# Kernel tuning notes

Hardware: AMD Instinct MI355X
Metric: run time of the kernel (lower is better)

Reference implementation:

```python
import jax, jax.numpy as jnp
import numpy as np

N = 40000      # nodes
E = 640000     # edges (before self-loops)
G = 64         # graphs in batch
H = 4          # heads
C = 64         # channels per head (graph_hidden_channels)
F_IN = 256     # num_node_features
NHID = 1024
NOUT = 768
NEG_SLOPE = 0.2


def setup_inputs() -> dict:
    key = jax.random.key(0)
    ks = jax.random.split(key, 20)
    s = 0.05
    inp = {
        "x": jax.random.normal(ks[0], (N, F_IN), jnp.float32),
        "edge_index": jax.random.randint(ks[1], (2, E), 0, N, dtype=jnp.int64),
        "batch": jnp.sort(jax.random.randint(ks[2], (N,), 0, G, dtype=jnp.int64)),
        # GATConv 1: in F_IN -> H heads x C
        "W1": jax.random.normal(ks[3], (F_IN, H * C), jnp.float32) * s,
        "as1": jax.random.normal(ks[4], (H, C), jnp.float32) * s,
        "ad1": jax.random.normal(ks[5], (H, C), jnp.float32) * s,
        "b1": jnp.zeros((H * C,), jnp.float32),
        # GATConv 2: in H*C -> H x C
        "W2": jax.random.normal(ks[6], (H * C, H * C), jnp.float32) * s,
        "as2": jax.random.normal(ks[7], (H, C), jnp.float32) * s,
        "ad2": jax.random.normal(ks[8], (H, C), jnp.float32) * s,
        "b2": jnp.zeros((H * C,), jnp.float32),
        # GATConv 3
        "W3": jax.random.normal(ks[9], (H * C, H * C), jnp.float32) * s,
        "as3": jax.random.normal(ks[10], (H, C), jnp.float32) * s,
        "ad3": jax.random.normal(ks[11], (H, C), jnp.float32) * s,
        "b3": jnp.zeros((H * C,), jnp.float32),
        # MLP head
        "Wm1": jax.random.normal(ks[12], (H * C, NHID), jnp.float32) * s,
        "bm1": jnp.zeros((NHID,), jnp.float32),
        "Wm2": jax.random.normal(ks[13], (NHID, NOUT), jnp.float32) * s,
        "bm2": jnp.zeros((NOUT,), jnp.float32),
    }
    return inp


def _gat_layer(x, src, dst, W, a_src, a_dst, b):
    """PyG GATConv (concat=True, self-loops already in src/dst)."""
    n = x.shape[0]
    h = (x @ W).reshape(n, H, C)                       # [N,H,C]
    # per-node attention scalars (gather scalars per edge, not full features)
    alpha_src = jnp.einsum('nhc,hc->nh', h, a_src)     # [N,H]
    alpha_dst = jnp.einsum('nhc,hc->nh', h, a_dst)     # [N,H]
    e = alpha_src[src] + alpha_dst[dst]                # [E,H]
    e = jax.nn.leaky_relu(e, NEG_SLOPE)
    # segment softmax over incoming edges of each dst node
    m = jax.ops.segment_max(e, dst, num_segments=n)    # [N,H]
    e = jnp.exp(e - m[dst])
    denom = jax.ops.segment_sum(e, dst, num_segments=n)  # [N,H]; >0 via self-loops
    alpha = e / denom[dst]                             # [E,H]
    # scatter-add weighted source features to destinations
    msg = h[src] * alpha[:, :, None]                   # [E,H,C]
    out = jax.ops.segment_sum(msg, dst, num_segments=n)  # [N,H,C]
    return out.reshape(n, H * C) + b


def reference(x, edge_index, batch,
              W1, as1, ad1, b1,
              W2, as2, ad2, b2,
              W3, as3, ad3, b3,
              Wm1, bm1, Wm2, bm2):
    n = x.shape[0]
    loops = jnp.arange(n, dtype=edge_index.dtype)
    src = jnp.concatenate([edge_index[0], loops])
    dst = jnp.concatenate([edge_index[1], loops])

    h = jax.nn.relu(_gat_layer(x, src, dst, W1, as1, ad1, b1))
    h = jax.nn.relu(_gat_layer(h, src, dst, W2, as2, ad2, b2))
    h = _gat_layer(h, src, dst, W3, as3, ad3, b3)

    # global mean pool over graphs
    sums = jax.ops.segment_sum(h, batch, num_segments=G)      # [G, H*C]
    counts = jax.ops.segment_sum(jnp.ones((n,), h.dtype), batch, num_segments=G)
    pooled = sums / jnp.maximum(counts, 1.0)[:, None]

    out = jax.nn.relu(pooled @ Wm1 + bm1)
    out = out @ Wm2 + bm2
    return out
```

## Files before the change

kernel.cpp:

```cpp
#include <hip/hip_runtime.h>
#include <hip/hip_bf16.h>
#include <math.h>

#define N_NODES 40000
#define N_EDGES 640000
#define N_GRAPH 64
#define HEADS 4
#define CHAN 64
#define HC 256
#define NHID 1024
#define NOUT 768
#define E_TOT (N_EDGES + N_NODES)
#define SCAN_NB ((N_NODES + 255) / 256)

typedef __attribute__((ext_vector_type(8))) short bf16x8;
typedef __attribute__((ext_vector_type(4))) float f32x4;

__device__ inline float bflo(unsigned u) { return __uint_as_float(u << 16); }
__device__ inline float bfhi(unsigned u) { return __uint_as_float(u & 0xffff0000u); }

__device__ inline unsigned bfbits(float f) {
    __hip_bfloat16 b = __float2bfloat16(f);
    return (unsigned)*reinterpret_cast<unsigned short*>(&b);
}
__device__ inline unsigned pk2bf(float lo, float hi) {
    return bfbits(lo) | (bfbits(hi) << 16);
}


__global__ void conv_wt3_kernel(const float* __restrict__ W1, const float* __restrict__ W2,
                                const float* __restrict__ W3, __hip_bfloat16* __restrict__ T1,
                                __hip_bfloat16* __restrict__ T2, __hip_bfloat16* __restrict__ T3) {
    const float* W = (blockIdx.y == 0) ? W1 : (blockIdx.y == 1) ? W2 : W3;
    __hip_bfloat16* T = (blockIdx.y == 0) ? T1 : (blockIdx.y == 1) ? T2 : T3;
    int k = blockIdx.x, n = threadIdx.x;
    T[(size_t)n * 256 + k] = __float2bfloat16(W[(size_t)k * 256 + n]);
}


__global__ void count_deg_kernel(const int* __restrict__ ei, int* __restrict__ deg) {
    int i = blockIdx.x * blockDim.x + threadIdx.x;
    if (i >= E_TOT) return;
    int dst = (i < N_EDGES) ? ei[N_EDGES + i] : (i - N_EDGES);
    atomicAdd(&deg[dst], 1);
}

__global__ __launch_bounds__(256)
void scan_p1_kernel(const int* __restrict__ deg, int* __restrict__ bsum) {
    const int b = blockIdx.x, t = threadIdx.x;
    const int i = b * 256 + t;
    int v = (i < N_NODES) ? deg[i] : 0;
    #pragma unroll
    for (int off = 1; off < 64; off <<= 1) v += __shfl_xor(v, off, 64);
    __shared__ int ws[4];
    if ((t & 63) == 0) ws[t >> 6] = v;
    __syncthreads();
    if (t == 0) bsum[b] = ws[0] + ws[1] + ws[2] + ws[3];
}

__global__ __launch_bounds__(256)
void scan_p2_kernel(int* __restrict__ bsum) {
    __shared__ int s[256];
    const int t = threadIdx.x;
    int v = (t < SCAN_NB) ? bsum[t] : 0;
    s[t] = v;
    __syncthreads();
    #pragma unroll
    for (int off = 1; off < 256; off <<= 1) {
        int x = (t >= off) ? s[t - off] : 0;
        __syncthreads();
        s[t] += x;
        __syncthreads();
    }
    if (t < SCAN_NB) bsum[t] = s[t] - v;
}

__global__ __launch_bounds__(256)
void scan_p3_kernel(const int* __restrict__ deg, const int* __restrict__ bsum,
                    int* __restrict__ rowptr) {
    __shared__ int s[256];
    const int b = blockIdx.x, t = threadIdx.x;
    const int i = b * 256 + t;
    int v = (i < N_NODES) ? deg[i] : 0;
    s[t] = v;
    __syncthreads();
    #pragma unroll
    for (int off = 1; off < 256; off <<= 1) {
        int x = (t >= off) ? s[t - off] : 0;
        __syncthreads();
        s[t] += x;
        __syncthreads();
    }
    if (i < N_NODES) rowptr[i] = bsum[b] + s[t] - v;
    if (i == 0) rowptr[N_NODES] = E_TOT;
}

__global__ void fill_csr_kernel(const int* __restrict__ ei, const int* __restrict__ rowptr,
                                int* __restrict__ cursor, int* __restrict__ csr_src) {
    int i = blockIdx.x * blockDim.x + threadIdx.x;
    if (i >= E_TOT) return;
    int src, dst;
    if (i < N_EDGES) { src = ei[i]; dst = ei[N_EDGES + i]; }
    else             { src = dst = i - N_EDGES; }
    int pos = atomicAdd(&cursor[dst], 1);
    csr_src[rowptr[dst] + pos] = src;
}


template<int CAST>
__global__ __launch_bounds__(256)
void gemm_mfma_kernel(const void* __restrict__ Ain, const __hip_bfloat16* __restrict__ Wt,
                      __hip_bfloat16* __restrict__ C,
                      const float* __restrict__ a_s, const float* __restrict__ a_d,
                      float* __restrict__ asrc, float* __restrict__ adst) {
    __shared__ __align__(16) union {
        struct { ushort A0[32][32]; ushort B0[256][32]; ushort A1[32][32]; ushort B1[256][32]; } t;
        float strip[4][16][68];
    } lds;

    const int tid = threadIdx.x;
    const int lane = tid & 63;
    const int l15 = lane & 15, lq = lane >> 4;
    const int wc  = tid >> 6;
    const int row0 = blockIdx.x * 32;
    const char* Wb = (const char*)Wt;
    const int br = tid >> 2;
    const int bq = tid & 3;

    f32x4 acc[2][4];
    #pragma unroll
    for (int m = 0; m < 2; m++)
        #pragma unroll
        for (int n = 0; n < 4; n++)
            acc[m][n] = (f32x4){0.f, 0.f, 0.f, 0.f};

    {
        #pragma unroll
        for (int c = 0; c < 4; c++) {
            uint4 v = *reinterpret_cast<const uint4*>(Wb + (size_t)(c * 64 + br) * 512 + bq * 16);
            *reinterpret_cast<uint4*>(&lds.t.B0[c * 64 + br][bq * 8]) = v;
        }
        if (CAST) {
            const float* Af = (const float*)Ain;
            float4 v = *reinterpret_cast<const float4*>(&Af[(size_t)(row0 + (tid >> 3)) * 256 + (tid & 7) * 4]);
            uint2 w = make_uint2(pk2bf(v.x, v.y), pk2bf(v.z, v.w));
            *reinterpret_cast<uint2*>((ushort*)lds.t.A0 + tid * 4) = w;
        } else if (tid < 128) {
            const char* Ab = (const char*)Ain;
            uint4 v = *reinterpret_cast<const uint4*>(Ab + (size_t)(row0 + (tid >> 2)) * 512 + (tid & 3) * 16);
            *reinterpret_cast<uint4*>((ushort*)lds.t.A0 + tid * 8) = v;
        }
        __syncthreads();
    }

    for (int kt = 0; kt < 8; ++kt) {
        ushort (*Acur)[32] = (kt & 1) ? lds.t.A1 : lds.t.A0;
        ushort (*Bcur)[32] = (kt & 1) ? lds.t.B1 : lds.t.B0;
        bf16x8 af[2], bfr[4];
        #pragma unroll
        for (int m = 0; m < 2; m++)
            af[m] = *reinterpret_cast<const bf16x8*>(&Acur[m * 16 + l15][lq * 8]);
        #pragma unroll
        for (int n = 0; n < 4; n++)
            bfr[n] = *reinterpret_cast<const bf16x8*>(&Bcur[wc * 64 + n * 16 + l15][lq * 8]);
        uint4 rb0, rb1, rb2, rb3, ra; float4 rf;
        if (kt < 7) {
            const size_t ko = (size_t)(kt + 1) * 64;
            rb0 = *reinterpret_cast<const uint4*>(Wb + (size_t)(      br) * 512 + bq * 16 + ko);
            rb1 = *reinterpret_cast<const uint4*>(Wb + (size_t)( 64 + br) * 512 + bq * 16 + ko);
            rb2 = *reinterpret_cast<const uint4*>(Wb + (size_t)(128 + br) * 512 + bq * 16 + ko);
            rb3 = *reinterpret_cast<const uint4*>(Wb + (size_t)(192 + br) * 512 + bq * 16 + ko);
            if (CAST) {
                const float* Af = (const float*)Ain;
                rf = *reinterpret_cast<const float4*>(&Af[(size_t)(row0 + (tid >> 3)) * 256 + (kt + 1) * 32 + (tid & 7) * 4]);
            } else if (tid < 128) {
                const char* Ab = (const char*)Ain;
                ra = *reinterpret_cast<const uint4*>(Ab + (size_t)(row0 + (tid >> 2)) * 512 + (tid & 3) * 16 + ko);
            }
        }
        #pragma unroll
        for (int m = 0; m < 2; m++)
            #pragma unroll
            for (int n = 0; n < 4; n++)
                acc[m][n] = __builtin_amdgcn_mfma_f32_16x16x32_bf16(af[m], bfr[n], acc[m][n], 0, 0, 0);
        if (kt < 7) {
            ushort (*Anx)[32] = (kt & 1) ? lds.t.A0 : lds.t.A1;
            ushort (*Bnx)[32] = (kt & 1) ? lds.t.B0 : lds.t.B1;
            *reinterpret_cast<uint4*>(&Bnx[      br][bq * 8]) = rb0;
            *reinterpret_cast<uint4*>(&Bnx[ 64 + br][bq * 8]) = rb1;
            *reinterpret_cast<uint4*>(&Bnx[128 + br][bq * 8]) = rb2;
            *reinterpret_cast<uint4*>(&Bnx[192 + br][bq * 8]) = rb3;
            if (CAST) {
                uint2 w = make_uint2(pk2bf(rf.x, rf.y), pk2bf(rf.z, rf.w));
                *reinterpret_cast<uint2*>((ushort*)Anx + tid * 4) = w;
            } else if (tid < 128) {
                *reinterpret_cast<uint4*>((ushort*)Anx + tid * 8) = ra;
            }
            __syncthreads();
        }
    }

    const int head = wc;
    const int r  = lane >> 2;
    const int cq = lane & 3;
    #pragma unroll
    for (int m = 0; m < 2; m++) {
        #pragma unroll
        for (int n = 0; n < 4; n++)
            #pragma unroll
            for (int reg = 0; reg < 4; reg++)
                lds.strip[wc][lq * 4 + reg][n * 16 + l15] = acc[m][n][reg];
        f32x4 c0 = *reinterpret_cast<const f32x4*>(&lds.strip[wc][r][cq * 16]);
        f32x4 c1 = *reinterpret_cast<const f32x4*>(&lds.strip[wc][r][cq * 16 + 4]);
        f32x4 c2 = *reinterpret_cast<const f32x4*>(&lds.strip[wc][r][cq * 16 + 8]);
        f32x4 c3 = *reinterpret_cast<const f32x4*>(&lds.strip[wc][r][cq * 16 + 12]);
        float ps = 0.f, pd = 0.f;
        #pragma unroll
        for (int k4 = 0; k4 < 4; k4++) {
            f32x4 cv = (k4 == 0) ? c0 : (k4 == 1) ? c1 : (k4 == 2) ? c2 : c3;
            #pragma unroll
            for (int j = 0; j < 4; j++) {
                ps = fmaf(cv[j], a_s[head * 64 + cq * 16 + k4 * 4 + j], ps);
                pd = fmaf(cv[j], a_d[head * 64 + cq * 16 + k4 * 4 + j], pd);
            }
        }
        ps += __shfl_xor(ps, 1, 4); ps += __shfl_xor(ps, 2, 4);
        pd += __shfl_xor(pd, 1, 4); pd += __shfl_xor(pd, 2, 4);
        const int row = row0 + m * 16 + r;
        if (cq == 0) {
            asrc[row * 4 + head] = ps;
            adst[row * 4 + head] = pd;
        }
        uint4 o0 = make_uint4(pk2bf(c0[0], c0[1]), pk2bf(c0[2], c0[3]),
                              pk2bf(c1[0], c1[1]), pk2bf(c1[2], c1[3]));
        uint4 o1 = make_uint4(pk2bf(c2[0], c2[1]), pk2bf(c2[2], c2[3]),
                              pk2bf(c3[0], c3[1]), pk2bf(c3[2], c3[3]));
        __hip_bfloat16* Cp = C + (size_t)row * 256 + wc * 64 + cq * 16;
        *reinterpret_cast<uint4*>(Cp) = o0;
        *reinterpret_cast<uint4*>(Cp + 8) = o1;
    }
}


#define ACHUNK 256

__global__ __launch_bounds__(256)
void gat_fused_agg(const __hip_bfloat16* __restrict__ h, const float* __restrict__ asrc,
                   const float* __restrict__ adst, const int* __restrict__ rowptr,
                   const int* __restrict__ csr_src, const float* __restrict__ bias,
                   __hip_bfloat16* __restrict__ out, int do_relu) {
    __shared__ int   s_src[ACHUNK];
    __shared__ float s_w[ACHUNK][5];
    __shared__ float s_acc[8][HC];
    __shared__ float s_sum[4];

    const int n = blockIdx.x;
    const int t = threadIdx.x;
    const int lane = t & 63;
    const int wid = t >> 6;
    const int grp = t >> 5;
    const int gl  = t & 31;
    const int h3  = gl >> 3;
    const int start = rowptr[n];
    const int deg = rowptr[n + 1] - start;
    const float ad = adst[n * 4 + wid];

    float ssum = 0.f;
    float acc[8] = {0.f, 0.f, 0.f, 0.f, 0.f, 0.f, 0.f, 0.f};

    for (int c0 = 0; c0 < deg; c0 += ACHUNK) {
        const int cn = min(ACHUNK, deg - c0);
        if (c0) __syncthreads();
        for (int e = lane; e < cn; e += 64) {
            int src = csr_src[start + c0 + e];
            if (wid == 0) s_src[e] = src;
            float sc = asrc[src * 4 + wid] + ad;
            sc = (sc >= 0.f) ? sc : 0.2f * sc;
            float w = __expf(sc);
            s_w[e][wid] = w;
            ssum += w;
        }
        __syncthreads();
        #pragma unroll 2
        for (int e = grp; e < cn; e += 8) {
            float w = s_w[e][h3];
            uint4 v = *reinterpret_cast<const uint4*>(&h[(size_t)s_src[e] * HC + gl * 8]);
            acc[0] = fmaf(w, bflo(v.x), acc[0]);
            acc[1] = fmaf(w, bfhi(v.x), acc[1]);
            acc[2] = fmaf(w, bflo(v.y), acc[2]);
            acc[3] = fmaf(w, bfhi(v.y), acc[3]);
            acc[4] = fmaf(w, bflo(v.z), acc[4]);
            acc[5] = fmaf(w, bfhi(v.z), acc[5]);
            acc[6] = fmaf(w, bflo(v.w), acc[6]);
            acc[7] = fmaf(w, bfhi(v.w), acc[7]);
        }
    }
    #pragma unroll
    for (int off = 1; off < 64; off <<= 1) ssum += __shfl_xor(ssum, off, 64);
    if (lane == 0) s_sum[wid] = ssum;
    *reinterpret_cast<float4*>(&s_acc[grp][gl * 8])     = make_float4(acc[0], acc[1], acc[2], acc[3]);
    *reinterpret_cast<float4*>(&s_acc[grp][gl * 8 + 4]) = make_float4(acc[4], acc[5], acc[6], acc[7]);
    __syncthreads();
    float tot = 0.f;
    #pragma unroll
    for (int g = 0; g < 8; g++) tot += s_acc[g][t];
    float r = tot / s_sum[t >> 6] + bias[t];
    if (do_relu) r = fmaxf(r, 0.f);
    out[(size_t)n * HC + t] = __float2bfloat16(r);
}


__global__ __launch_bounds__(1024)
void pool_mlp1_kernel(const __hip_bfloat16* __restrict__ h, const int* __restrict__ batch,
                      const float* __restrict__ Wm1, const float* __restrict__ bm1,
                      float* __restrict__ hidden) {
    __shared__ float s_part[4][256];
    __shared__ float row[256];
    const int g = blockIdx.x, t = threadIdx.x;
    int lo = 0, hi = N_NODES;
    while (lo < hi) { int mid = (lo + hi) >> 1; if (batch[mid] < g) lo = mid + 1; else hi = mid; }
    const int start = lo;
    lo = 0; hi = N_NODES;
    while (lo < hi) { int mid = (lo + hi) >> 1; if (batch[mid] < g + 1) lo = mid + 1; else hi = mid; }
    const int end = lo;

    const int sub = t >> 8, ch = t & 255;
    float a = 0.f;
    for (int n = start + sub; n < end; n += 4)
        a += __bfloat162float(h[(size_t)n * HC + ch]);
    s_part[sub][ch] = a;
    __syncthreads();
    if (t < 256) {
        float c = (float)max(end - start, 1);
        row[t] = (s_part[0][t] + s_part[1][t] + s_part[2][t] + s_part[3][t]) / c;
    }
    __syncthreads();
    float acc = bm1[t];
    for (int k = 0; k < 256; k++) acc = fmaf(row[k], Wm1[(size_t)k * NHID + t], acc);
    hidden[(size_t)g * NHID + t] = fmaxf(acc, 0.f);
}

__global__ __launch_bounds__(768)
void mlp2_kernel(const float* __restrict__ hidden, const float* __restrict__ W,
                 const float* __restrict__ b, float* __restrict__ out) {
    __shared__ float row[NHID];
    const int g = blockIdx.x, t = threadIdx.x;
    row[t] = hidden[g * NHID + t];
    if (t < NHID - NOUT) row[NOUT + t] = hidden[g * NHID + NOUT + t];
    __syncthreads();
    float acc = b[t];
    for (int k = 0; k < NHID; k++) acc = fmaf(row[k], W[(size_t)k * NOUT + t], acc);
    out[g * NOUT + t] = acc;
}


extern "C" void kernel_launch(void* const* d_in, const int* in_sizes, int n_in,
                              void* d_out, int out_size, void* d_ws, size_t ws_size,
                              hipStream_t stream) {
    const float* x  = (const float*)d_in[0];
    const int* ei   = (const int*)d_in[1];
    const int* batch = (const int*)d_in[2];
    const float* W1 = (const float*)d_in[3];
    const float* as1 = (const float*)d_in[4];
    const float* ad1 = (const float*)d_in[5];
    const float* b1 = (const float*)d_in[6];
    const float* W2 = (const float*)d_in[7];
    const float* as2 = (const float*)d_in[8];
    const float* ad2 = (const float*)d_in[9];
    const float* b2 = (const float*)d_in[10];
    const float* W3 = (const float*)d_in[11];
    const float* as3 = (const float*)d_in[12];
    const float* ad3 = (const float*)d_in[13];
    const float* b3 = (const float*)d_in[14];
    const float* Wm1 = (const float*)d_in[15];
    const float* bm1 = (const float*)d_in[16];
    const float* Wm2 = (const float*)d_in[17];
    const float* bm2 = (const float*)d_in[18];
    float* out = (float*)d_out;

    char* base = (char*)d_ws;
    size_t off = 0;
    auto alloc = [&](size_t bytes) { char* p = base + off; off = (off + bytes + 255) & ~(size_t)255; return p; };
    __hip_bfloat16* hA   = (__hip_bfloat16*)alloc((size_t)N_NODES * 256 * 2);
    __hip_bfloat16* hB   = (__hip_bfloat16*)alloc((size_t)N_NODES * 256 * 2);
    __hip_bfloat16* Wt1  = (__hip_bfloat16*)alloc((size_t)256 * 256 * 2);
    __hip_bfloat16* Wt2  = (__hip_bfloat16*)alloc((size_t)256 * 256 * 2);
    __hip_bfloat16* Wt3  = (__hip_bfloat16*)alloc((size_t)256 * 256 * 2);
    float* asrc   = (float*)alloc((size_t)N_NODES * 4 * 4);
    float* adst   = (float*)alloc((size_t)N_NODES * 4 * 4);
    int*   deg    = (int*)alloc((size_t)N_NODES * 4);
    int*   cursor = (int*)alloc((size_t)N_NODES * 4);
    int*   rowptr = (int*)alloc((size_t)(N_NODES + 1) * 4);
    int*   bsum   = (int*)alloc((size_t)SCAN_NB * 4);
    int*   csrsrc = (int*)alloc((size_t)E_TOT * 4);
    float* hidden = (float*)alloc((size_t)N_GRAPH * NHID * 4);
    (void)ws_size; (void)n_in; (void)in_sizes; (void)out_size;

    hipMemsetAsync(deg, 0, (size_t)N_NODES * 4 * 2, stream);

    conv_wt3_kernel<<<dim3(256, 3), 256, 0, stream>>>(W1, W2, W3, Wt1, Wt2, Wt3);

    const int eb = (E_TOT + 255) / 256;
    count_deg_kernel<<<eb, 256, 0, stream>>>(ei, deg);
    scan_p1_kernel<<<SCAN_NB, 256, 0, stream>>>(deg, bsum);
    scan_p2_kernel<<<1, 256, 0, stream>>>(bsum);
    scan_p3_kernel<<<SCAN_NB, 256, 0, stream>>>(deg, bsum, rowptr);
    fill_csr_kernel<<<eb, 256, 0, stream>>>(ei, rowptr, cursor, csrsrc);

    const int ggrid = N_NODES / 32;

    gemm_mfma_kernel<1><<<ggrid, 256, 0, stream>>>(x, Wt1, hA, as1, ad1, asrc, adst);
    gat_fused_agg<<<N_NODES, 256, 0, stream>>>(hA, asrc, adst, rowptr, csrsrc, b1, hB, 1);
    gemm_mfma_kernel<0><<<ggrid, 256, 0, stream>>>(hB, Wt2, hA, as2, ad2, asrc, adst);
    gat_fused_agg<<<N_NODES, 256, 0, stream>>>(hA, asrc, adst, rowptr, csrsrc, b2, hB, 1);
    gemm_mfma_kernel<0><<<ggrid, 256, 0, stream>>>(hB, Wt3, hA, as3, ad3, asrc, adst);
    gat_fused_agg<<<N_NODES, 256, 0, stream>>>(hA, asrc, adst, rowptr, csrsrc, b3, hB, 0);

    pool_mlp1_kernel<<<N_GRAPH, 1024, 0, stream>>>(hB, batch, Wm1, bm1, hidden);
    mlp2_kernel<<<N_GRAPH, NOUT, 0, stream>>>(hidden, Wm2, bm2, out);
}
```

Measured before the change: 422.1 us.

## Keep weight slice in registers and stream A rows directly in GEMM

The node-feature GEMM is restructured so each 512-thread block loads a 128-column weight slice once into swizzled LDS and then into registers, covering two heads. Each wave streams 16-row A tiles straight from global memory into registers with a prefetch of the next tile, with no per-k LDS staging and no __syncthreads in the main loop. The attention dot products are computed from MFMA outputs with cross-lane shuffles instead of an LDS transpose. The aim is to cut LDS traffic and synchronization, at the cost of heavy register pressure (64 B fragments per lane) and a small grid of 250 blocks.

```diff
diff --git a/kernel.cpp b/kernel.cpp
--- a/kernel.cpp
+++ b/kernel.cpp
@@ -108,136 +108,122 @@
 
 
 template<int CAST>
-__global__ __launch_bounds__(256)
+__global__ __launch_bounds__(512, 2)
 void gemm_mfma_kernel(const void* __restrict__ Ain, const __hip_bfloat16* __restrict__ Wt,
                       __hip_bfloat16* __restrict__ C,
                       const float* __restrict__ a_s, const float* __restrict__ a_d,
                       float* __restrict__ asrc, float* __restrict__ adst) {
-    __shared__ __align__(16) union {
-        struct { ushort A0[32][32]; ushort B0[256][32]; ushort A1[32][32]; ushort B1[256][32]; } t;
-        float strip[4][16][68];
-    } lds;
+    __shared__ ushort Wl[128 * 256];
 
     const int tid = threadIdx.x;
     const int lane = tid & 63;
     const int l15 = lane & 15, lq = lane >> 4;
-    const int wc  = tid >> 6;
-    const int row0 = blockIdx.x * 32;
-    const char* Wb = (const char*)Wt;
-    const int br = tid >> 2;
-    const int bq = tid & 3;
-
-    f32x4 acc[2][4];
-    #pragma unroll
-    for (int m = 0; m < 2; m++)
-        #pragma unroll
-        for (int n = 0; n < 4; n++)
-            acc[m][n] = (f32x4){0.f, 0.f, 0.f, 0.f};
+    const int w = tid >> 6;
+    const int hsel = w >> 2;
+    const int stripe = w & 3;
+    const int head = blockIdx.y * 2 + hsel;
+    const int row_base = blockIdx.x * 320;
 
     {
-        #pragma unroll
-        for (int c = 0; c < 4; c++) {
-            uint4 v = *reinterpret_cast<const uint4*>(Wb + (size_t)(c * 64 + br) * 512 + bq * 16);
-            *reinterpret_cast<uint4*>(&lds.t.B0[c * 64 + br][bq * 8]) = v;
-        }
+        const int col = tid >> 2;
+        const char* Wb = (const char*)(Wt + (size_t)(blockIdx.y * 128 + col) * 256);
+        #pragma unroll
+        for (int j = 0; j < 8; j++) {
+            int q = (tid & 3) * 8 + j;
+            uint4 v = *reinterpret_cast<const uint4*>(Wb + q * 16);
+            *reinterpret_cast<uint4*>(&Wl[col * 256 + ((q ^ (col & 7)) * 8)]) = v;
+        }
+    }
+    __syncthreads();
+
+    bf16x8 b[8][4];
+    #pragma unroll
+    for (int kt = 0; kt < 8; kt++)
+        #pragma unroll
+        for (int n = 0; n < 4; n++) {
+            int cl = hsel * 64 + n * 16 + l15;
+            int q = kt * 4 + lq;
+            b[kt][n] = *reinterpret_cast<const bf16x8*>(&Wl[cl * 256 + ((q ^ (cl & 7)) * 8)]);
+        }
+
+    float was[4], wad[4];
+    #pragma unroll
+    for (int n = 0; n < 4; n++) {
+        was[n] = a_s[head * 64 + n * 16 + l15];
+        wad[n] = a_d[head * 64 + n * 16 + l15];
+    }
+
+    auto loadA = [&](int T, bf16x8* a) {
+        const int row = row_base + T * 16 + l15;
         if (CAST) {
             const float* Af = (const float*)Ain;
-            float4 v = *reinterpret_cast<const float4*>(&Af[(size_t)(row0 + (tid >> 3)) * 256 + (tid & 7) * 4]);
-            uint2 w = make_uint2(pk2bf(v.x, v.y), pk2bf(v.z, v.w));
-            *reinterpret_cast<uint2*>((ushort*)lds.t.A0 + tid * 4) = w;
-        } else if (tid < 128) {
-            const char* Ab = (const char*)Ain;
-            uint4 v = *reinterpret_cast<const uint4*>(Ab + (size_t)(row0 + (tid >> 2)) * 512 + (tid & 3) * 16);
-            *reinterpret_cast<uint4*>((ushort*)lds.t.A0 + tid * 8) = v;
-        }
-        __syncthreads();
-    }
-
-    for (int kt = 0; kt < 8; ++kt) {
-        ushort (*Acur)[32] = (kt & 1) ? lds.t.A1 : lds.t.A0;
-        ushort (*Bcur)[32] = (kt & 1) ? lds.t.B1 : lds.t.B0;
-        bf16x8 af[2], bfr[4];
-        #pragma unroll
-        for (int m = 0; m < 2; m++)
-            af[m] = *reinterpret_cast<const bf16x8*>(&Acur[m * 16 + l15][lq * 8]);
+            #pragma unroll
+            for (int kt = 0; kt < 8; kt++) {
+                float4 u0 = *reinterpret_cast<const float4*>(&Af[(size_t)row * 256 + kt * 32 + lq * 8]);
+                float4 u1 = *reinterpret_cast<const float4*>(&Af[(size_t)row * 256 + kt * 32 + lq * 8 + 4]);
+                uint4 uv = make_uint4(pk2bf(u0.x, u0.y), pk2bf(u0.z, u0.w),
+                                      pk2bf(u1.x, u1.y), pk2bf(u1.z, u1.w));
+                a[kt] = *reinterpret_cast<bf16x8*>(&uv);
+            }
+        } else {
+            const __hip_bfloat16* Ab = (const __hip_bfloat16*)Ain;
+            #pragma unroll
+            for (int kt = 0; kt < 8; kt++) {
+                uint4 uv = *reinterpret_cast<const uint4*>(&Ab[(size_t)row * 256 + kt * 32 + lq * 8]);
+                a[kt] = *reinterpret_cast<bf16x8*>(&uv);
+            }
+        }
+    };
+
+    bf16x8 aA[8], aB[8];
+    loadA(stripe, aA);
+    #pragma unroll
+    for (int ti = 0; ti < 5; ti++) {
+        const int T = stripe + ti * 4;
+        if (ti < 4) loadA(T + 4, aB);
+        f32x4 acc[4];
+        #pragma unroll
+        for (int n = 0; n < 4; n++) acc[n] = (f32x4){0.f, 0.f, 0.f, 0.f};
+        #pragma unroll
+        for (int kt = 0; kt < 8; kt++)
+            #pragma unroll
+            for (int n = 0; n < 4; n++)
+                acc[n] = __builtin_amdgcn_mfma_f32_16x16x32_bf16(aA[kt], b[kt][n], acc[n], 0, 0, 0);
+
+        #pragma unroll
+        for (int reg = 0; reg < 4; reg++) {
+            float ps = 0.f, pd = 0.f;
+            #pragma unroll
+            for (int n = 0; n < 4; n++) {
+                float v = acc[n][reg];
+                ps = fmaf(v, was[n], ps);
+                pd = fmaf(v, wad[n], pd);
+            }
+            #pragma unroll
+            for (int off = 1; off < 16; off <<= 1) {
+                ps += __shfl_xor(ps, off, 16);
+                pd += __shfl_xor(pd, off, 16);
+            }
+            const int row = row_base + T * 16 + lq * 4 + reg;
+            if (l15 == 0) {
+                asrc[row * 4 + head] = ps;
+                adst[row * 4 + head] = pd;
+            }
+        }
         #pragma unroll
         for (int n = 0; n < 4; n++)
-            bfr[n] = *reinterpret_cast<const bf16x8*>(&Bcur[wc * 64 + n * 16 + l15][lq * 8]);
-        uint4 rb0, rb1, rb2, rb3, ra; float4 rf;
-        if (kt < 7) {
-            const size_t ko = (size_t)(kt + 1) * 64;
-            rb0 = *reinterpret_cast<const uint4*>(Wb + (size_t)(      br) * 512 + bq * 16 + ko);
-            rb1 = *reinterpret_cast<const uint4*>(Wb + (size_t)( 64 + br) * 512 + bq * 16 + ko);
-            rb2 = *reinterpret_cast<const uint4*>(Wb + (size_t)(128 + br) * 512 + bq * 16 + ko);
-            rb3 = *reinterpret_cast<const uint4*>(Wb + (size_t)(192 + br) * 512 + bq * 16 + ko);
-            if (CAST) {
-                const float* Af = (const float*)Ain;
-                rf = *reinterpret_cast<const float4*>(&Af[(size_t)(row0 + (tid >> 3)) * 256 + (kt + 1) * 32 + (tid & 7) * 4]);
-            } else if (tid < 128) {
-                const char* Ab = (const char*)Ain;
-                ra = *reinterpret_cast<const uint4*>(Ab + (size_t)(row0 + (tid >> 2)) * 512 + (tid & 3) * 16 + ko);
-            }
-        }
-        #pragma unroll
-        for (int m = 0; m < 2; m++)
-            #pragma unroll
-            for (int n = 0; n < 4; n++)
-                acc[m][n] = __builtin_amdgcn_mfma_f32_16x16x32_bf16(af[m], bfr[n], acc[m][n], 0, 0, 0);
-        if (kt < 7) {
-            ushort (*Anx)[32] = (kt & 1) ? lds.t.A0 : lds.t.A1;
-            ushort (*Bnx)[32] = (kt & 1) ? lds.t.B0 : lds.t.B1;
-            *reinterpret_cast<uint4*>(&Bnx[      br][bq * 8]) = rb0;
-            *reinterpret_cast<uint4*>(&Bnx[ 64 + br][bq * 8]) = rb1;
-            *reinterpret_cast<uint4*>(&Bnx[128 + br][bq * 8]) = rb2;
-            *reinterpret_cast<uint4*>(&Bnx[192 + br][bq * 8]) = rb3;
-            if (CAST) {
-                uint2 w = make_uint2(pk2bf(rf.x, rf.y), pk2bf(rf.z, rf.w));
-                *reinterpret_cast<uint2*>((ushort*)Anx + tid * 4) = w;
-            } else if (tid < 128) {
-                *reinterpret_cast<uint4*>((ushort*)Anx + tid * 8) = ra;
-            }
-            __syncthreads();
-        }
-    }
-
-    const int head = wc;
-    const int r  = lane >> 2;
-    const int cq = lane & 3;
-    #pragma unroll
-    for (int m = 0; m < 2; m++) {
-        #pragma unroll
-        for (int n = 0; n < 4; n++)
-            #pragma unroll
-            for (int reg = 0; reg < 4; reg++)
-                lds.strip[wc][lq * 4 + reg][n * 16 + l15] = acc[m][n][reg];
-        f32x4 c0 = *reinterpret_cast<const f32x4*>(&lds.strip[wc][r][cq * 16]);
-        f32x4 c1 = *reinterpret_cast<const f32x4*>(&lds.strip[wc][r][cq * 16 + 4]);
-        f32x4 c2 = *reinterpret_cast<const f32x4*>(&lds.strip[wc][r][cq * 16 + 8]);
-        f32x4 c3 = *reinterpret_cast<const f32x4*>(&lds.strip[wc][r][cq * 16 + 12]);
-        float ps = 0.f, pd = 0.f;
-        #pragma unroll
-        for (int k4 = 0; k4 < 4; k4++) {
-            f32x4 cv = (k4 == 0) ? c0 : (k4 == 1) ? c1 : (k4 == 2) ? c2 : c3;
-            #pragma unroll
-            for (int j = 0; j < 4; j++) {
-                ps = fmaf(cv[j], a_s[head * 64 + cq * 16 + k4 * 4 + j], ps);
-                pd = fmaf(cv[j], a_d[head * 64 + cq * 16 + k4 * 4 + j], pd);
-            }
-        }
-        ps += __shfl_xor(ps, 1, 4); ps += __shfl_xor(ps, 2, 4);
-        pd += __shfl_xor(pd, 1, 4); pd += __shfl_xor(pd, 2, 4);
-        const int row = row0 + m * 16 + r;
-        if (cq == 0) {
-            asrc[row * 4 + head] = ps;
-            adst[row * 4 + head] = pd;
-        }
-        uint4 o0 = make_uint4(pk2bf(c0[0], c0[1]), pk2bf(c0[2], c0[3]),
-                              pk2bf(c1[0], c1[1]), pk2bf(c1[2], c1[3]));
-        uint4 o1 = make_uint4(pk2bf(c2[0], c2[1]), pk2bf(c2[2], c2[3]),
-                              pk2bf(c3[0], c3[1]), pk2bf(c3[2], c3[3]));
-        __hip_bfloat16* Cp = C + (size_t)row * 256 + wc * 64 + cq * 16;
-        *reinterpret_cast<uint4*>(Cp) = o0;
-        *reinterpret_cast<uint4*>(Cp + 8) = o1;
+            #pragma unroll
+            for (int reg = 0; reg < 4; reg++) {
+                float v = acc[n][reg];
+                float vp = __shfl_xor(v, 1, 16);
+                const int row = row_base + T * 16 + lq * 4 + reg;
+                if (!(l15 & 1)) {
+                    unsigned pk = pk2bf(v, vp);
+                    *reinterpret_cast<unsigned*>(&C[(size_t)row * 256 + head * 64 + n * 16 + l15]) = pk;
+                }
+            }
+        #pragma unroll
+        for (int kk = 0; kk < 8; kk++) aA[kk] = aB[kk];
     }
 }
 
@@ -407,13 +393,13 @@
     scan_p3_kernel<<<SCAN_NB, 256, 0, stream>>>(deg, bsum, rowptr);
     fill_csr_kernel<<<eb, 256, 0, stream>>>(ei, rowptr, cursor, csrsrc);
 
-    const int ggrid = N_NODES / 32;
-
-    gemm_mfma_kernel<1><<<ggrid, 256, 0, stream>>>(x, Wt1, hA, as1, ad1, asrc, adst);
+    const dim3 ggrid(125, 2);
+
+    gemm_mfma_kernel<1><<<ggrid, 512, 0, stream>>>(x, Wt1, hA, as1, ad1, asrc, adst);
     gat_fused_agg<<<N_NODES, 256, 0, stream>>>(hA, asrc, adst, rowptr, csrsrc, b1, hB, 1);
-    gemm_mfma_kernel<0><<<ggrid, 256, 0, stream>>>(hB, Wt2, hA, as2, ad2, asrc, adst);
+    gemm_mfma_kernel<0><<<ggrid, 512, 0, stream>>>(hB, Wt2, hA, as2, ad2, asrc, adst);
     gat_fused_agg<<<N_NODES, 256, 0, stream>>>(hA, asrc, adst, rowptr, csrsrc, b2, hB, 1);
-    gemm_mfma_kernel<0><<<ggrid, 256, 0, stream>>>(hB, Wt3, hA, as3, ad3, asrc, adst);
+    gemm_mfma_kernel<0><<<ggrid, 512, 0, stream>>>(hB, Wt3, hA, as3, ad3, asrc, adst);
     gat_fused_agg<<<N_NODES, 256, 0, stream>>>(hA, asrc, adst, rowptr, csrsrc, b3, hB, 0);
 
     pool_mlp1_kernel<<<N_GRAPH, 1024, 0, stream>>>(hB, batch, Wm1, bm1, hidden);
```

Result: slower. 431.6 us, median of 2 (+2.2%).
